# Optimization experiments

Hardware: AMD Instinct MI355X
Metric: run time of the kernel (lower is better)

## Reference

```python
import jax, jax.numpy as jnp
import numpy as np

NEARZERO = 1e-5
# Bounds for the 14 parameters consumed by the HBV step, in order:
# BETA, FC, K0, K1, K2, LP, PERC, UZL, TT, CFMAX, CFR, CWH, BETAET, C
BOUNDS = np.array([
    [1.0, 6.0], [50.0, 1000.0], [0.05, 0.9], [0.01, 0.5], [0.001, 0.2],
    [0.2, 1.0], [0.0, 10.0], [0.0, 100.0], [-2.5, 2.5], [0.5, 10.0],
    [0.0, 0.1], [0.0, 0.2], [0.3, 5.0], [0.0, 1.0]], dtype=np.float32)

T, G = 365, 50000


def setup_inputs() -> dict:
    key = jax.random.key(0)
    k1, k2, k3, k4 = jax.random.split(key, 4)
    precip = jax.random.uniform(k1, (T, G), dtype=jnp.float32) * 10.0   # mm/day
    temp = jax.random.normal(k2, (T, G), dtype=jnp.float32) * 10.0      # degC
    pet = jax.random.uniform(k3, (T, G), dtype=jnp.float32) * 5.0       # mm/day
    phy_params = jax.random.uniform(k4, (G, 14), dtype=jnp.float32)     # normalized [0,1]
    return {"precip": precip, "temp": temp, "pet": pet, "phy_params": phy_params}


def _hbv2_scan(precip, temp, pet, phy_params):
    lo = jnp.asarray(BOUNDS[:, 0])
    hi = jnp.asarray(BOUNDS[:, 1])
    p = lo + phy_params * (hi - lo)  # descale, [G, 14]
    (BETA, FC, K0, K1, K2, LP, PERC_p, UZL, TT, CFMAX, CFR, CWH, BETAET, C) = [p[:, i] for i in range(14)]

    def step(state, forc):
        SNOWPACK, MELTWATER, SM, SUZ, SLZ = state
        pr, tm, pe = forc
        is_rain = (tm >= TT).astype(jnp.float32)
        RAIN = pr * is_rain
        SNOW = pr * (1.0 - is_rain)
        SNOWPACK = SNOWPACK + SNOW
        melt = jnp.minimum(jnp.maximum(CFMAX * (tm - TT), 0.0), SNOWPACK)
        MELTWATER = MELTWATER + melt
        SNOWPACK = SNOWPACK - melt
        refreezing = jnp.minimum(jnp.maximum(CFR * CFMAX * (TT - tm), 0.0), MELTWATER)
        SNOWPACK = SNOWPACK + refreezing
        MELTWATER = MELTWATER - refreezing
        tosoil = jnp.maximum(MELTWATER - CWH * SNOWPACK, 0.0)
        MELTWATER = MELTWATER - tosoil
        soil_wetness = jnp.clip((SM / FC) ** BETA, 0.0, 1.0)
        recharge = (RAIN + tosoil) * soil_wetness
        SM = SM + RAIN + tosoil - recharge
        excess = jnp.maximum(SM - FC, 0.0)
        SM = SM - excess
        evapfactor = jnp.clip((SM / (LP * FC)) ** BETAET, 0.0, 1.0)
        ETact = jnp.minimum(SM, pe * evapfactor)
        SM = jnp.maximum(SM - ETact, NEARZERO)
        capillary = jnp.minimum(SLZ, C * SLZ * (1.0 - jnp.minimum(SM / FC, 1.0)))
        SM = jnp.maximum(SM + capillary, NEARZERO)
        SLZ = jnp.maximum(SLZ - capillary, NEARZERO)
        SUZ = SUZ + recharge + excess
        PERC = jnp.minimum(SUZ, PERC_p)
        SUZ = SUZ - PERC
        Q0 = K0 * jnp.maximum(SUZ - UZL, 0.0)
        SUZ = SUZ - Q0
        Q1 = K1 * SUZ
        SUZ = SUZ - Q1
        SLZ = jnp.maximum(SLZ + PERC, 0.0)
        Q2 = K2 * SLZ
        SLZ = SLZ - Q2
        return (SNOWPACK, MELTWATER, SM, SUZ, SLZ), Q0 + Q1 + Q2

    init = tuple(jnp.full((precip.shape[1],), NEARZERO, dtype=jnp.float32) for _ in range(5))
    _, Q = jax.lax.scan(step, init, (precip, temp, pet))
    return Q  # [T, G] total streamflow per timestep per basin


def reference(precip, temp, pet, phy_params):
    return _hbv2_scan(precip, temp, pet, phy_params)
```

## Files before the change

kernel.cpp:

```cpp
#include <hip/hip_runtime.h>

#define NZ 1e-5f
#define TC 16

__device__ __forceinline__ float fast_exp2(float x) {
#if __has_builtin(__builtin_amdgcn_exp2f)
    return __builtin_amdgcn_exp2f(x);
#else
    return exp2f(x);
#endif
}

__device__ __forceinline__ float fast_log2(float x) {
#if __has_builtin(__builtin_amdgcn_logf)
    return __builtin_amdgcn_logf(x);
#else
    return log2f(x);
#endif
}

__device__ __forceinline__ void gload_lds16(const float* src, float* dst_lds) {
    __builtin_amdgcn_global_load_lds(
        (const __attribute__((address_space(1))) void*)src,
        (__attribute__((address_space(3))) void*)dst_lds,
        16, 0, 0);
}

__global__ __launch_bounds__(64, 1) void hbv_kernel(
    const float* __restrict__ precip,
    const float* __restrict__ temp,
    const float* __restrict__ pet,
    const float* __restrict__ phy,
    float* __restrict__ out,
    int G, int T)
{
    __shared__ float lds[2][3][TC][64];

    const int lane = threadIdx.x;
    const int g0   = blockIdx.x * 64;
    const int g    = g0 + lane;
    const bool valid = (g < G);
    const int gp   = valid ? g : (G - 1);

    const float lo[14] = {1.0f, 50.0f, 0.05f, 0.01f, 0.001f, 0.2f, 0.0f,
                          0.0f, -2.5f, 0.5f, 0.0f, 0.0f, 0.3f, 0.0f};
    const float hi[14] = {6.0f, 1000.0f, 0.9f, 0.5f, 0.2f, 1.0f, 10.0f,
                          100.0f, 2.5f, 10.0f, 0.1f, 0.2f, 5.0f, 1.0f};
    float p[14];
#pragma unroll
    for (int i = 0; i < 14; ++i)
        p[i] = lo[i] + phy[gp * 14 + i] * (hi[i] - lo[i]);

    const float BETA = p[0], FC = p[1], K0 = p[2], K1 = p[3], K2 = p[4];
    const float LP = p[5], PERCp = p[6], UZL = p[7], TT = p[8], CFMAX = p[9];
    const float CFR = p[10], CWH = p[11], BETAET = p[12], C = p[13];
    const float invFC   = 1.0f / FC;
    const float invLPFC = 1.0f / (LP * FC);
    const float CFRX    = CFR * CFMAX;

    float SP = NZ, MW = NZ, SM = NZ, SUZ = NZ, SLZ = NZ;

    auto hbv_step = [&](float pr, float tm, float pe) -> float {
        const float RAIN = (tm >= TT) ? pr : 0.0f;
        const float SNOW = pr - RAIN;
        SP += SNOW;
        float melt = fminf(fmaxf(CFMAX * (tm - TT), 0.0f), SP);
        MW += melt;
        SP -= melt;
        float refr = fminf(fmaxf(CFRX * (TT - tm), 0.0f), MW);
        SP += refr;
        MW -= refr;
        float tosoil = fmaxf(MW - CWH * SP, 0.0f);
        MW -= tosoil;
        float sw = fminf(fast_exp2(BETA * fast_log2(SM * invFC)), 1.0f);
        float rt = RAIN + tosoil;
        float recharge = rt * sw;
        SM += rt - recharge;
        float excess = fmaxf(SM - FC, 0.0f);
        SM -= excess;
        float ef = fminf(fast_exp2(BETAET * fast_log2(SM * invLPFC)), 1.0f);
        float ETact = fminf(SM, pe * ef);
        SM = fmaxf(SM - ETact, NZ);
        float cap = fminf(SLZ, C * SLZ * (1.0f - fminf(SM * invFC, 1.0f)));
        SM = fmaxf(SM + cap, NZ);
        SLZ = fmaxf(SLZ - cap, NZ);
        SUZ += recharge + excess;
        float PERC = fminf(SUZ, PERCp);
        SUZ -= PERC;
        float Q0 = K0 * fmaxf(SUZ - UZL, 0.0f);
        SUZ -= Q0;
        float Q1 = K1 * SUZ;
        SUZ -= Q1;
        SLZ = fmaxf(SLZ + PERC, 0.0f);
        float Q2 = K2 * SLZ;
        SLZ -= Q2;
        return Q0 + Q1 + Q2;
    };

    if ((G & 3) == 0) {
        const int rsub = lane >> 4;
        const int csub = (lane & 15) << 2;
        int gcol = g0 + csub;
        if (gcol > G - 4) gcol = G - 4;

        const int nt = (T + TC - 1) / TC;

        auto issue_tile = [&](int k, int b) {
            const int t0 = k * TC;
#pragma unroll
            for (int q = 0; q < TC / 4; ++q) {
                int t = t0 + 4 * q + rsub;
                if (t > T - 1) t = T - 1;
                const size_t off = (size_t)t * G + gcol;
                gload_lds16(precip + off, &lds[b][0][4 * q][0]);
                gload_lds16(temp   + off, &lds[b][1][4 * q][0]);
                gload_lds16(pet    + off, &lds[b][2][4 * q][0]);
            }
        };

        issue_tile(0, 0);
        asm volatile("s_waitcnt vmcnt(0)" ::: "memory");
        __builtin_amdgcn_sched_barrier(0);

        for (int k = 0; k < nt; ++k) {
            const int b = k & 1;
            if (k + 1 < nt) {
                issue_tile(k + 1, b ^ 1);
                __builtin_amdgcn_sched_barrier(0);
            }
            const int t0 = k * TC;
#pragma unroll
            for (int j = 0; j < TC; ++j) {
                const int t = t0 + j;
                const float pr = lds[b][0][j][lane];
                const float tm = lds[b][1][j][lane];
                const float pe = lds[b][2][j][lane];
                const float q = hbv_step(pr, tm, pe);
                if (valid && t < T)
                    out[(size_t)t * G + g] = q;
            }
            if (k + 1 < nt) {
                asm volatile("s_waitcnt vmcnt(12)" ::: "memory");
                __builtin_amdgcn_sched_barrier(0);
            }
        }
    } else {
        for (int t = 0; t < T; ++t) {
            const size_t idx = (size_t)t * G + gp;
            const float q = hbv_step(precip[idx], temp[idx], pet[idx]);
            if (valid) out[idx] = q;
        }
    }
}

extern "C" void kernel_launch(void* const* d_in, const int* in_sizes, int n_in,
                              void* d_out, int out_size, void* d_ws, size_t ws_size,
                              hipStream_t stream) {
    const float* precip = (const float*)d_in[0];
    const float* temp   = (const float*)d_in[1];
    const float* pet    = (const float*)d_in[2];
    const float* phy    = (const float*)d_in[3];
    float* out = (float*)d_out;

    const int G = in_sizes[3] / 14;
    const int T = in_sizes[0] / G;

    dim3 block(64);
    dim3 grid((G + 63) / 64);
    hbv_kernel<<<grid, block, 0, stream>>>(precip, temp, pet, phy, out, G, T);
}
```

Measured before the change: 257.0 us.

## Process two basins per thread to expose ILP and widen stores

Each thread now carries two independent basin state chains, interleaving their serial recurrences so the dependent-latency chain of each step can overlap. Blocks cover 128 basins, LDS tiles widen accordingly, loads use float2 LDS reads and float2 global stores, and the wait count is adjusted for the doubled per-tile load count. This halves the grid to about 391 waves on a device with many CUs, reducing occupancy/parallelism while raising register pressure. A partial last block now waits for all loads conservatively.

```diff
diff --git a/kernel.cpp b/kernel.cpp
--- a/kernel.cpp
+++ b/kernel.cpp
@@ -2,6 +2,7 @@
 
 #define NZ 1e-5f
 #define TC 16
+#define NB 2
 
 __device__ __forceinline__ float fast_exp2(float x) {
 #if __has_builtin(__builtin_amdgcn_exp2f)
@@ -34,87 +35,107 @@
     float* __restrict__ out,
     int G, int T)
 {
-    __shared__ float lds[2][3][TC][64];
+    __shared__ float lds[2][3][TC][64 * NB];
 
     const int lane = threadIdx.x;
-    const int g0   = blockIdx.x * 64;
-    const int g    = g0 + lane;
-    const bool valid = (g < G);
-    const int gp   = valid ? g : (G - 1);
+    const int g0   = blockIdx.x * (64 * NB);
+
+    bool vb[NB];
+    int  gb[NB];
+#pragma unroll
+    for (int c = 0; c < NB; ++c) {
+        const int g = g0 + NB * lane + c;
+        vb[c] = (g < G);
+        gb[c] = vb[c] ? g : (G - 1);
+    }
 
     const float lo[14] = {1.0f, 50.0f, 0.05f, 0.01f, 0.001f, 0.2f, 0.0f,
                           0.0f, -2.5f, 0.5f, 0.0f, 0.0f, 0.3f, 0.0f};
     const float hi[14] = {6.0f, 1000.0f, 0.9f, 0.5f, 0.2f, 1.0f, 10.0f,
                           100.0f, 2.5f, 10.0f, 0.1f, 0.2f, 5.0f, 1.0f};
-    float p[14];
-#pragma unroll
-    for (int i = 0; i < 14; ++i)
-        p[i] = lo[i] + phy[gp * 14 + i] * (hi[i] - lo[i]);
-
-    const float BETA = p[0], FC = p[1], K0 = p[2], K1 = p[3], K2 = p[4];
-    const float LP = p[5], PERCp = p[6], UZL = p[7], TT = p[8], CFMAX = p[9];
-    const float CFR = p[10], CWH = p[11], BETAET = p[12], C = p[13];
-    const float invFC   = 1.0f / FC;
-    const float invLPFC = 1.0f / (LP * FC);
-    const float CFRX    = CFR * CFMAX;
-
-    float SP = NZ, MW = NZ, SM = NZ, SUZ = NZ, SLZ = NZ;
-
-    auto hbv_step = [&](float pr, float tm, float pe) -> float {
+
+    float P[NB][14];
+#pragma unroll
+    for (int c = 0; c < NB; ++c)
+#pragma unroll
+        for (int i = 0; i < 14; ++i)
+            P[c][i] = lo[i] + phy[gb[c] * 14 + i] * (hi[i] - lo[i]);
+
+    float invFC_[NB], invLPFC_[NB], CFRX_[NB];
+#pragma unroll
+    for (int c = 0; c < NB; ++c) {
+        invFC_[c]   = 1.0f / P[c][1];
+        invLPFC_[c] = 1.0f / (P[c][5] * P[c][1]);
+        CFRX_[c]    = P[c][10] * P[c][9];
+    }
+
+    float SP[NB], MW[NB], SM[NB], SUZ[NB], SLZ[NB];
+#pragma unroll
+    for (int c = 0; c < NB; ++c) {
+        SP[c] = NZ; MW[c] = NZ; SM[c] = NZ; SUZ[c] = NZ; SLZ[c] = NZ;
+    }
+
+    auto hbv_step = [&](int c, float pr, float tm, float pe) -> float {
+        const float BETA = P[c][0], FC = P[c][1], K0 = P[c][2], K1 = P[c][3];
+        const float K2 = P[c][4], PERCp = P[c][6], UZL = P[c][7], TT = P[c][8];
+        const float CFMAX = P[c][9], CWH = P[c][11], BETAET = P[c][12], C = P[c][13];
+        const float invFC = invFC_[c], invLPFC = invLPFC_[c], CFRX = CFRX_[c];
+
         const float RAIN = (tm >= TT) ? pr : 0.0f;
         const float SNOW = pr - RAIN;
-        SP += SNOW;
-        float melt = fminf(fmaxf(CFMAX * (tm - TT), 0.0f), SP);
-        MW += melt;
-        SP -= melt;
-        float refr = fminf(fmaxf(CFRX * (TT - tm), 0.0f), MW);
-        SP += refr;
-        MW -= refr;
-        float tosoil = fmaxf(MW - CWH * SP, 0.0f);
-        MW -= tosoil;
-        float sw = fminf(fast_exp2(BETA * fast_log2(SM * invFC)), 1.0f);
+        SP[c] += SNOW;
+        float melt = fminf(fmaxf(CFMAX * (tm - TT), 0.0f), SP[c]);
+        MW[c] += melt;
+        SP[c] -= melt;
+        float refr = fminf(fmaxf(CFRX * (TT - tm), 0.0f), MW[c]);
+        SP[c] += refr;
+        MW[c] -= refr;
+        float tosoil = fmaxf(MW[c] - CWH * SP[c], 0.0f);
+        MW[c] -= tosoil;
+        float sw = fminf(fast_exp2(BETA * fast_log2(SM[c] * invFC)), 1.0f);
         float rt = RAIN + tosoil;
         float recharge = rt * sw;
-        SM += rt - recharge;
-        float excess = fmaxf(SM - FC, 0.0f);
-        SM -= excess;
-        float ef = fminf(fast_exp2(BETAET * fast_log2(SM * invLPFC)), 1.0f);
-        float ETact = fminf(SM, pe * ef);
-        SM = fmaxf(SM - ETact, NZ);
-        float cap = fminf(SLZ, C * SLZ * (1.0f - fminf(SM * invFC, 1.0f)));
-        SM = fmaxf(SM + cap, NZ);
-        SLZ = fmaxf(SLZ - cap, NZ);
-        SUZ += recharge + excess;
-        float PERC = fminf(SUZ, PERCp);
-        SUZ -= PERC;
-        float Q0 = K0 * fmaxf(SUZ - UZL, 0.0f);
-        SUZ -= Q0;
-        float Q1 = K1 * SUZ;
-        SUZ -= Q1;
-        SLZ = fmaxf(SLZ + PERC, 0.0f);
-        float Q2 = K2 * SLZ;
-        SLZ -= Q2;
+        SM[c] += rt - recharge;
+        float excess = fmaxf(SM[c] - FC, 0.0f);
+        SM[c] -= excess;
+        float ef = fminf(fast_exp2(BETAET * fast_log2(SM[c] * invLPFC)), 1.0f);
+        float ETact = fminf(SM[c], pe * ef);
+        SM[c] = fmaxf(SM[c] - ETact, NZ);
+        float cap = fminf(SLZ[c], C * SLZ[c] * (1.0f - fminf(SM[c] * invFC, 1.0f)));
+        SM[c] = fmaxf(SM[c] + cap, NZ);
+        SLZ[c] = fmaxf(SLZ[c] - cap, NZ);
+        SUZ[c] += recharge + excess;
+        float PERC = fminf(SUZ[c], PERCp);
+        SUZ[c] -= PERC;
+        float Q0 = K0 * fmaxf(SUZ[c] - UZL, 0.0f);
+        SUZ[c] -= Q0;
+        float Q1 = K1 * SUZ[c];
+        SUZ[c] -= Q1;
+        SLZ[c] = fmaxf(SLZ[c] + PERC, 0.0f);
+        float Q2 = K2 * SLZ[c];
+        SLZ[c] -= Q2;
         return Q0 + Q1 + Q2;
     };
 
     if ((G & 3) == 0) {
-        const int rsub = lane >> 4;
-        const int csub = (lane & 15) << 2;
+        const int rsub = lane >> 5;
+        const int csub = (lane & 31) << 2;
         int gcol = g0 + csub;
         if (gcol > G - 4) gcol = G - 4;
 
         const int nt = (T + TC - 1) / TC;
+        const bool full = (g0 + 64 * NB <= G);
 
         auto issue_tile = [&](int k, int b) {
             const int t0 = k * TC;
 #pragma unroll
-            for (int q = 0; q < TC / 4; ++q) {
-                int t = t0 + 4 * q + rsub;
+            for (int q = 0; q < TC / 2; ++q) {
+                int t = t0 + 2 * q + rsub;
                 if (t > T - 1) t = T - 1;
                 const size_t off = (size_t)t * G + gcol;
-                gload_lds16(precip + off, &lds[b][0][4 * q][0]);
-                gload_lds16(temp   + off, &lds[b][1][4 * q][0]);
-                gload_lds16(pet    + off, &lds[b][2][4 * q][0]);
+                gload_lds16(precip + off, &lds[b][0][2 * q][0]);
+                gload_lds16(temp   + off, &lds[b][1][2 * q][0]);
+                gload_lds16(pet    + off, &lds[b][2][2 * q][0]);
             }
         };
 
@@ -132,23 +153,39 @@
 #pragma unroll
             for (int j = 0; j < TC; ++j) {
                 const int t = t0 + j;
-                const float pr = lds[b][0][j][lane];
-                const float tm = lds[b][1][j][lane];
-                const float pe = lds[b][2][j][lane];
-                const float q = hbv_step(pr, tm, pe);
-                if (valid && t < T)
-                    out[(size_t)t * G + g] = q;
+                const float2 prv = *(const float2*)&lds[b][0][j][NB * lane];
+                const float2 tmv = *(const float2*)&lds[b][1][j][NB * lane];
+                const float2 pev = *(const float2*)&lds[b][2][j][NB * lane];
+                const float q0 = hbv_step(0, prv.x, tmv.x, pev.x);
+                const float q1 = hbv_step(1, prv.y, tmv.y, pev.y);
+                if (t < T) {
+                    const size_t idx = (size_t)t * G + (g0 + NB * lane);
+                    if (vb[1])
+                        *(float2*)&out[idx] = make_float2(q0, q1);
+                    else if (vb[0])
+                        out[idx] = q0;
+                }
             }
             if (k + 1 < nt) {
-                asm volatile("s_waitcnt vmcnt(12)" ::: "memory");
+                if (full) {
+                    asm volatile("s_waitcnt vmcnt(16)" ::: "memory");
+                } else {
+                    asm volatile("s_waitcnt vmcnt(0)" ::: "memory");
+                }
                 __builtin_amdgcn_sched_barrier(0);
             }
         }
     } else {
         for (int t = 0; t < T; ++t) {
-            const size_t idx = (size_t)t * G + gp;
-            const float q = hbv_step(precip[idx], temp[idx], pet[idx]);
-            if (valid) out[idx] = q;
+            float q[NB];
+#pragma unroll
+            for (int c = 0; c < NB; ++c) {
+                const size_t idx = (size_t)t * G + gb[c];
+                q[c] = hbv_step(c, precip[idx], temp[idx], pet[idx]);
+            }
+#pragma unroll
+            for (int c = 0; c < NB; ++c)
+                if (vb[c]) out[(size_t)t * G + gb[c]] = q[c];
         }
     }
 }
@@ -166,6 +203,6 @@
     const int T = in_sizes[0] / G;
 
     dim3 block(64);
-    dim3 grid((G + 63) / 64);
+    dim3 grid((G + 64 * NB - 1) / (64 * NB));
     hbv_kernel<<<grid, block, 0, stream>>>(precip, temp, pet, phy, out, G, T);
 }
```

After: 299.5 us. 1.17x slower.

## Software-pipeline snow and soil phases across timesteps with LDS prefetch

Applied to the files above, without the earlier changes.

Splits the HBV step into a snow phase and a soil phase. The snow phase of step t+1 is run alongside the soil phase of step t, so the two independent dependency chains can interleave and hide ALU and transcendental latency on the serial recurrence. LDS reads are also loaded two steps ahead, and the wait for the next tile is moved so the last two steps of each tile read from the freshly loaded buffer. The tail tile is handled in a separate loop. This adds register pressure and more complex indexing, and the pipelined path now requires at least two tiles of timesteps.

```diff
diff --git a/kernel.cpp b/kernel.cpp
--- a/kernel.cpp
+++ b/kernel.cpp
@@ -57,10 +57,11 @@
     const float invFC   = 1.0f / FC;
     const float invLPFC = 1.0f / (LP * FC);
     const float CFRX    = CFR * CFMAX;
+    (void)LP; (void)CFR;
 
     float SP = NZ, MW = NZ, SM = NZ, SUZ = NZ, SLZ = NZ;
 
-    auto hbv_step = [&](float pr, float tm, float pe) -> float {
+    auto snow_phase = [&](float pr, float tm) -> float {
         const float RAIN = (tm >= TT) ? pr : 0.0f;
         const float SNOW = pr - RAIN;
         SP += SNOW;
@@ -72,8 +73,11 @@
         MW -= refr;
         float tosoil = fmaxf(MW - CWH * SP, 0.0f);
         MW -= tosoil;
+        return RAIN + tosoil;
+    };
+
+    auto soil_phase = [&](float rt, float pe) -> float {
         float sw = fminf(fast_exp2(BETA * fast_log2(SM * invFC)), 1.0f);
-        float rt = RAIN + tosoil;
         float recharge = rt * sw;
         SM += rt - recharge;
         float excess = fmaxf(SM - FC, 0.0f);
@@ -97,13 +101,14 @@
         return Q0 + Q1 + Q2;
     };
 
-    if ((G & 3) == 0) {
+    if (((G & 3) == 0) && (T >= 2 * TC)) {
         const int rsub = lane >> 4;
         const int csub = (lane & 15) << 2;
         int gcol = g0 + csub;
         if (gcol > G - 4) gcol = G - 4;
 
         const int nt = (T + TC - 1) / TC;
+        const int FT = nt - 1;
 
         auto issue_tile = [&](int k, int b) {
             const int t0 = k * TC;
@@ -118,36 +123,85 @@
             }
         };
 
+        float* outp = out + (size_t)g;
+
         issue_tile(0, 0);
         asm volatile("s_waitcnt vmcnt(0)" ::: "memory");
         __builtin_amdgcn_sched_barrier(0);
 
-        for (int k = 0; k < nt; ++k) {
-            const int b = k & 1;
-            if (k + 1 < nt) {
-                issue_tile(k + 1, b ^ 1);
-                __builtin_amdgcn_sched_barrier(0);
-            }
-            const int t0 = k * TC;
-#pragma unroll
-            for (int j = 0; j < TC; ++j) {
-                const int t = t0 + j;
-                const float pr = lds[b][0][j][lane];
-                const float tm = lds[b][1][j][lane];
-                const float pe = lds[b][2][j][lane];
-                const float q = hbv_step(pr, tm, pe);
-                if (valid && t < T)
-                    out[(size_t)t * G + g] = q;
-            }
-            if (k + 1 < nt) {
-                asm volatile("s_waitcnt vmcnt(12)" ::: "memory");
-                __builtin_amdgcn_sched_barrier(0);
-            }
+        float rt0, pe0, prN, tmN, peN;
+        {
+            const float prF = lds[0][0][0][lane];
+            const float tmF = lds[0][1][0][lane];
+            const float peF = lds[0][2][0][lane];
+            rt0 = snow_phase(prF, tmF);
+            pe0 = peF;
+            prN = lds[0][0][1][lane];
+            tmN = lds[0][1][1][lane];
+            peN = lds[0][2][1][lane];
+        }
+
+        for (int k = 0; k < FT; ++k) {
+            const int b = k & 1, nb = b ^ 1;
+            issue_tile(k + 1, nb);
+            __builtin_amdgcn_sched_barrier(0);
+
+#pragma unroll
+            for (int j = 0; j < TC - 2; ++j) {
+                const float prR = lds[b][0][j + 2][lane];
+                const float tmR = lds[b][1][j + 2][lane];
+                const float peR = lds[b][2][j + 2][lane];
+                const float rt1 = snow_phase(prN, tmN);
+                const float pe1 = peN;
+                const float q = soil_phase(rt0, pe0);
+                if (valid) *outp = q;
+                outp += G;
+                rt0 = rt1; pe0 = pe1;
+                prN = prR; tmN = tmR; peN = peR;
+            }
+
+            asm volatile("s_waitcnt vmcnt(14)" ::: "memory");
+            __builtin_amdgcn_sched_barrier(0);
+
+#pragma unroll
+            for (int j = TC - 2; j < TC; ++j) {
+                const float prR = lds[nb][0][j - (TC - 2)][lane];
+                const float tmR = lds[nb][1][j - (TC - 2)][lane];
+                const float peR = lds[nb][2][j - (TC - 2)][lane];
+                const float rt1 = snow_phase(prN, tmN);
+                const float pe1 = peN;
+                const float q = soil_phase(rt0, pe0);
+                if (valid) *outp = q;
+                outp += G;
+                rt0 = rt1; pe0 = pe1;
+                prN = prR; tmN = tmR; peN = peR;
+            }
+        }
+
+        {
+            const int b = FT & 1;
+            const int TAIL = T - FT * TC;
+            for (int j = 0; j + 1 < TAIL; ++j) {
+                const bool rd = (j + 2) < TAIL;
+                const float prR = rd ? lds[b][0][j + 2][lane] : 0.0f;
+                const float tmR = rd ? lds[b][1][j + 2][lane] : 0.0f;
+                const float peR = rd ? lds[b][2][j + 2][lane] : 0.0f;
+                const float rt1 = snow_phase(prN, tmN);
+                const float pe1 = peN;
+                const float q = soil_phase(rt0, pe0);
+                if (valid) *outp = q;
+                outp += G;
+                rt0 = rt1; pe0 = pe1;
+                prN = prR; tmN = tmR; peN = peR;
+            }
+            const float q = soil_phase(rt0, pe0);
+            if (valid) *outp = q;
         }
     } else {
         for (int t = 0; t < T; ++t) {
             const size_t idx = (size_t)t * G + gp;
-            const float q = hbv_step(precip[idx], temp[idx], pet[idx]);
+            const float rt = snow_phase(precip[idx], temp[idx]);
+            const float q = soil_phase(rt, pet[idx]);
             if (valid) out[idx] = q;
         }
     }
```

Result: no change. 253.2 us (-1.5%).

## Split HBV step into snow and soil wavefronts pipelined through LDS

Applied to the files above, without the earlier changes.

Each block now has two wavefronts. Wave 0 loads the forcing tiles and runs the snow routine, writing rain+tosoil and pet into an LDS buffer. Wave 1 runs the soil and groundwater routine one tile behind and writes the output. This splits the serial per-basin dependency chain across two waves so both stages can run in parallel on the SIMDs. The cost is a block barrier per tile and extra LDS traffic, and it doubles the threads per block over the same number of blocks.

```diff
diff --git a/kernel.cpp b/kernel.cpp
--- a/kernel.cpp
+++ b/kernel.cpp
@@ -26,7 +26,7 @@
         16, 0, 0);
 }
 
-__global__ __launch_bounds__(64, 1) void hbv_kernel(
+__global__ __launch_bounds__(128, 1) void hbv_kernel(
     const float* __restrict__ precip,
     const float* __restrict__ temp,
     const float* __restrict__ pet,
@@ -34,9 +34,12 @@
     float* __restrict__ out,
     int G, int T)
 {
-    __shared__ float lds[2][3][TC][64];
-
-    const int lane = threadIdx.x;
+    __shared__ float  ftile[2][3][TC][64];
+    __shared__ float2 rtpe[2][TC][64];
+
+    const int tid  = threadIdx.x;
+    const int lane = tid & 63;
+    const int wv   = tid >> 6;
     const int g0   = blockIdx.x * 64;
     const int g    = g0 + lane;
     const bool valid = (g < G);
@@ -46,109 +49,187 @@
                           0.0f, -2.5f, 0.5f, 0.0f, 0.0f, 0.3f, 0.0f};
     const float hi[14] = {6.0f, 1000.0f, 0.9f, 0.5f, 0.2f, 1.0f, 10.0f,
                           100.0f, 2.5f, 10.0f, 0.1f, 0.2f, 5.0f, 1.0f};
-    float p[14];
-#pragma unroll
-    for (int i = 0; i < 14; ++i)
-        p[i] = lo[i] + phy[gp * 14 + i] * (hi[i] - lo[i]);
-
-    const float BETA = p[0], FC = p[1], K0 = p[2], K1 = p[3], K2 = p[4];
-    const float LP = p[5], PERCp = p[6], UZL = p[7], TT = p[8], CFMAX = p[9];
-    const float CFR = p[10], CWH = p[11], BETAET = p[12], C = p[13];
-    const float invFC   = 1.0f / FC;
-    const float invLPFC = 1.0f / (LP * FC);
-    const float CFRX    = CFR * CFMAX;
-
-    float SP = NZ, MW = NZ, SM = NZ, SUZ = NZ, SLZ = NZ;
-
-    auto hbv_step = [&](float pr, float tm, float pe) -> float {
-        const float RAIN = (tm >= TT) ? pr : 0.0f;
-        const float SNOW = pr - RAIN;
-        SP += SNOW;
-        float melt = fminf(fmaxf(CFMAX * (tm - TT), 0.0f), SP);
-        MW += melt;
-        SP -= melt;
-        float refr = fminf(fmaxf(CFRX * (TT - tm), 0.0f), MW);
-        SP += refr;
-        MW -= refr;
-        float tosoil = fmaxf(MW - CWH * SP, 0.0f);
-        MW -= tosoil;
-        float sw = fminf(fast_exp2(BETA * fast_log2(SM * invFC)), 1.0f);
-        float rt = RAIN + tosoil;
-        float recharge = rt * sw;
-        SM += rt - recharge;
-        float excess = fmaxf(SM - FC, 0.0f);
-        SM -= excess;
-        float ef = fminf(fast_exp2(BETAET * fast_log2(SM * invLPFC)), 1.0f);
-        float ETact = fminf(SM, pe * ef);
-        SM = fmaxf(SM - ETact, NZ);
-        float cap = fminf(SLZ, C * SLZ * (1.0f - fminf(SM * invFC, 1.0f)));
-        SM = fmaxf(SM + cap, NZ);
-        SLZ = fmaxf(SLZ - cap, NZ);
-        SUZ += recharge + excess;
-        float PERC = fminf(SUZ, PERCp);
-        SUZ -= PERC;
-        float Q0 = K0 * fmaxf(SUZ - UZL, 0.0f);
-        SUZ -= Q0;
-        float Q1 = K1 * SUZ;
-        SUZ -= Q1;
-        SLZ = fmaxf(SLZ + PERC, 0.0f);
-        float Q2 = K2 * SLZ;
-        SLZ -= Q2;
-        return Q0 + Q1 + Q2;
-    };
-
-    if ((G & 3) == 0) {
-        const int rsub = lane >> 4;
-        const int csub = (lane & 15) << 2;
-        int gcol = g0 + csub;
-        if (gcol > G - 4) gcol = G - 4;
-
+
+    const bool fastp = ((G & 3) == 0) && (T >= 2 * TC);
+
+    if (fastp) {
         const int nt = (T + TC - 1) / TC;
 
-        auto issue_tile = [&](int k, int b) {
-            const int t0 = k * TC;
-#pragma unroll
-            for (int q = 0; q < TC / 4; ++q) {
-                int t = t0 + 4 * q + rsub;
-                if (t > T - 1) t = T - 1;
-                const size_t off = (size_t)t * G + gcol;
-                gload_lds16(precip + off, &lds[b][0][4 * q][0]);
-                gload_lds16(temp   + off, &lds[b][1][4 * q][0]);
-                gload_lds16(pet    + off, &lds[b][2][4 * q][0]);
+        if (wv == 0) {
+            float p[14];
+#pragma unroll
+            for (int i = 0; i < 14; ++i)
+                p[i] = lo[i] + phy[gp * 14 + i] * (hi[i] - lo[i]);
+            const float TT = p[8], CFMAX = p[9], CWH = p[11];
+            const float CFRX = p[10] * p[9];
+            float SP = NZ, MW = NZ;
+
+            const int rsub = lane >> 4;
+            const int csub = (lane & 15) << 2;
+            int gcol = g0 + csub;
+            if (gcol > G - 4) gcol = G - 4;
+
+            auto issue_tile = [&](int k, int b) {
+                const int t0 = k * TC;
+#pragma unroll
+                for (int q = 0; q < TC / 4; ++q) {
+                    int t = t0 + 4 * q + rsub;
+                    if (t > T - 1) t = T - 1;
+                    const size_t off = (size_t)t * G + gcol;
+                    gload_lds16(precip + off, &ftile[b][0][4 * q][0]);
+                    gload_lds16(temp   + off, &ftile[b][1][4 * q][0]);
+                    gload_lds16(pet    + off, &ftile[b][2][4 * q][0]);
+                }
+            };
+
+            issue_tile(0, 0);
+
+            for (int ph = 0; ph <= nt; ++ph) {
+                if (ph < nt) {
+                    const int b = ph & 1;
+                    if (ph + 1 < nt) {
+                        issue_tile(ph + 1, b ^ 1);
+                        asm volatile("s_waitcnt vmcnt(12)" ::: "memory");
+                    } else {
+                        asm volatile("s_waitcnt vmcnt(0)" ::: "memory");
+                    }
+                    __builtin_amdgcn_sched_barrier(0);
+#pragma unroll
+                    for (int j = 0; j < TC; ++j) {
+                        const float pr = ftile[b][0][j][lane];
+                        const float tm = ftile[b][1][j][lane];
+                        const float pe = ftile[b][2][j][lane];
+                        const float RAIN = (tm >= TT) ? pr : 0.0f;
+                        const float SNOW = pr - RAIN;
+                        SP += SNOW;
+                        float melt = fminf(fmaxf(CFMAX * (tm - TT), 0.0f), SP);
+                        MW += melt;
+                        SP -= melt;
+                        float refr = fminf(fmaxf(CFRX * (TT - tm), 0.0f), MW);
+                        SP += refr;
+                        MW -= refr;
+                        float tosoil = fmaxf(MW - CWH * SP, 0.0f);
+                        MW -= tosoil;
+                        rtpe[b][j][lane] = make_float2(RAIN + tosoil, pe);
+                    }
+                    asm volatile("s_waitcnt lgkmcnt(0)" ::: "memory");
+                    __builtin_amdgcn_sched_barrier(0);
+                }
+                __builtin_amdgcn_s_barrier();
+                asm volatile("" ::: "memory");
             }
-        };
-
-        issue_tile(0, 0);
-        asm volatile("s_waitcnt vmcnt(0)" ::: "memory");
-        __builtin_amdgcn_sched_barrier(0);
-
-        for (int k = 0; k < nt; ++k) {
-            const int b = k & 1;
-            if (k + 1 < nt) {
-                issue_tile(k + 1, b ^ 1);
-                __builtin_amdgcn_sched_barrier(0);
-            }
-            const int t0 = k * TC;
-#pragma unroll
-            for (int j = 0; j < TC; ++j) {
-                const int t = t0 + j;
-                const float pr = lds[b][0][j][lane];
-                const float tm = lds[b][1][j][lane];
-                const float pe = lds[b][2][j][lane];
-                const float q = hbv_step(pr, tm, pe);
-                if (valid && t < T)
-                    out[(size_t)t * G + g] = q;
-            }
-            if (k + 1 < nt) {
-                asm volatile("s_waitcnt vmcnt(12)" ::: "memory");
-                __builtin_amdgcn_sched_barrier(0);
+        } else {
+            float p[14];
+#pragma unroll
+            for (int i = 0; i < 14; ++i)
+                p[i] = lo[i] + phy[gp * 14 + i] * (hi[i] - lo[i]);
+            const float BETA = p[0], FC = p[1], K0 = p[2], K1 = p[3], K2 = p[4];
+            const float PERCp = p[6], UZL = p[7], BETAET = p[12], C = p[13];
+            const float invFC   = 1.0f / FC;
+            const float invLPFC = 1.0f / (p[5] * FC);
+            float SM = NZ, SUZ = NZ, SLZ = NZ;
+
+            auto soil_step = [&](float rt, float pe) -> float {
+                float sw = fminf(fast_exp2(BETA * fast_log2(SM * invFC)), 1.0f);
+                float recharge = rt * sw;
+                SM += rt - recharge;
+                float excess = fmaxf(SM - FC, 0.0f);
+                SM -= excess;
+                float ef = fminf(fast_exp2(BETAET * fast_log2(SM * invLPFC)), 1.0f);
+                float ETact = fminf(SM, pe * ef);
+                SM = fmaxf(SM - ETact, NZ);
+                float cap = fminf(SLZ, C * SLZ * (1.0f - fminf(SM * invFC, 1.0f)));
+                SM = fmaxf(SM + cap, NZ);
+                SLZ = fmaxf(SLZ - cap, NZ);
+                SUZ += recharge + excess;
+                float PERC = fminf(SUZ, PERCp);
+                SUZ -= PERC;
+                float Q0 = K0 * fmaxf(SUZ - UZL, 0.0f);
+                SUZ -= Q0;
+                float Q1 = K1 * SUZ;
+                SUZ -= Q1;
+                SLZ = fmaxf(SLZ + PERC, 0.0f);
+                float Q2 = K2 * SLZ;
+                SLZ -= Q2;
+                return Q0 + Q1 + Q2;
+            };
+
+            for (int ph = 0; ph <= nt; ++ph) {
+                if (ph >= 1) {
+                    const int c = ph - 1;
+                    const int b = c & 1;
+                    const int t0 = c * TC;
+                    const int steps = (t0 + TC <= T) ? TC : (T - t0);
+                    if (steps == TC) {
+                        float2 v = rtpe[b][0][lane];
+#pragma unroll
+                        for (int j = 0; j < TC; ++j) {
+                            const float2 vn = (j + 1 < TC)
+                                ? rtpe[b][j + 1][lane] : make_float2(0.f, 0.f);
+                            const float q = soil_step(v.x, v.y);
+                            if (valid) out[(size_t)(t0 + j) * G + g] = q;
+                            v = vn;
+                        }
+                    } else {
+                        for (int j = 0; j < steps; ++j) {
+                            const float2 v = rtpe[b][j][lane];
+                            const float q = soil_step(v.x, v.y);
+                            if (valid) out[(size_t)(t0 + j) * G + g] = q;
+                        }
+                    }
+                }
+                __builtin_amdgcn_s_barrier();
+                asm volatile("" ::: "memory");
             }
         }
     } else {
-        for (int t = 0; t < T; ++t) {
-            const size_t idx = (size_t)t * G + gp;
-            const float q = hbv_step(precip[idx], temp[idx], pet[idx]);
-            if (valid) out[idx] = q;
+        if (wv == 0) {
+            float p[14];
+#pragma unroll
+            for (int i = 0; i < 14; ++i)
+                p[i] = lo[i] + phy[gp * 14 + i] * (hi[i] - lo[i]);
+            const float BETA = p[0], FC = p[1], K0 = p[2], K1 = p[3], K2 = p[4];
+            const float PERCp = p[6], UZL = p[7], TT = p[8], CFMAX = p[9];
+            const float CWH = p[11], BETAET = p[12], C = p[13];
+            const float invFC = 1.0f / FC, invLPFC = 1.0f / (p[5] * FC);
+            const float CFRX = p[10] * p[9];
+            float SP = NZ, MW = NZ, SM = NZ, SUZ = NZ, SLZ = NZ;
+            for (int t = 0; t < T; ++t) {
+                const size_t idx = (size_t)t * G + gp;
+                const float pr = precip[idx], tm = temp[idx], pe = pet[idx];
+                const float RAIN = (tm >= TT) ? pr : 0.0f;
+                const float SNOW = pr - RAIN;
+                SP += SNOW;
+                float melt = fminf(fmaxf(CFMAX * (tm - TT), 0.0f), SP);
+                MW += melt; SP -= melt;
+                float refr = fminf(fmaxf(CFRX * (TT - tm), 0.0f), MW);
+                SP += refr; MW -= refr;
+                float tosoil = fmaxf(MW - CWH * SP, 0.0f);
+                MW -= tosoil;
+                float sw = fminf(fast_exp2(BETA * fast_log2(SM * invFC)), 1.0f);
+                float rt = RAIN + tosoil;
+                float recharge = rt * sw;
+                SM += rt - recharge;
+                float excess = fmaxf(SM - FC, 0.0f);
+                SM -= excess;
+                float ef = fminf(fast_exp2(BETAET * fast_log2(SM * invLPFC)), 1.0f);
+                float ETact = fminf(SM, pe * ef);
+                SM = fmaxf(SM - ETact, NZ);
+                float cap = fminf(SLZ, C * SLZ * (1.0f - fminf(SM * invFC, 1.0f)));
+                SM = fmaxf(SM + cap, NZ);
+                SLZ = fmaxf(SLZ - cap, NZ);
+                SUZ += recharge + excess;
+                float PERC = fminf(SUZ, PERCp);
+                SUZ -= PERC;
+                float Q0 = K0 * fmaxf(SUZ - UZL, 0.0f);
+                SUZ -= Q0;
+                float Q1 = K1 * SUZ;
+                SUZ -= Q1;
+                SLZ = fmaxf(SLZ + PERC, 0.0f);
+                float Q2 = K2 * SLZ;
+                SLZ -= Q2;
+                if (valid) out[idx] = Q0 + Q1 + Q2;
+            }
         }
     }
 }
@@ -165,7 +246,7 @@
     const int G = in_sizes[3] / 14;
     const int T = in_sizes[0] / G;
 
-    dim3 block(64);
+    dim3 block(128);
     dim3 grid((G + 63) / 64);
     hbv_kernel<<<grid, block, 0, stream>>>(precip, temp, pet, phy, out, G, T);
 }
```

New measurement: 252.4 us. No clear change (-1.8%).
